# Performance work log

Hardware: AMD Instinct MI355X
Metric: run time of the kernel (lower is better)

## Reference

```python
import jax, jax.numpy as jnp
import numpy as np

N, K, C, S = 32768, 16, 64, 8
EPS = 1e-5

def _bn(x, g, b):
    # BatchNorm1d in training mode: normalize over all axes except channel (last)
    axes = tuple(range(x.ndim - 1))
    m = x.mean(axes, keepdims=True)
    v = x.var(axes, keepdims=True)
    return (x - m) * jax.lax.rsqrt(v + EPS) * g + b

def setup_inputs() -> dict:
    key = jax.random.key(0)
    ks = jax.random.split(key, 24)
    def W(k, i, o):
        return (jax.random.normal(k, (i, o), jnp.float32) * 0.02)
    d = {}
    d['xyz'] = jax.random.normal(ks[0], (N, 3), jnp.float32)
    d['features'] = jax.random.normal(ks[1], (N, C), jnp.float32)
    d['velocities'] = jax.random.normal(ks[2], (N, 1), jnp.float32)
    # q/k/v projections
    d['wq'] = W(ks[3], C, C); d['bq'] = jnp.zeros((C,), jnp.float32)
    d['wk'] = W(ks[4], C, C); d['bk'] = jnp.zeros((C,), jnp.float32)
    d['wv'] = W(ks[5], C, C); d['bv'] = jnp.zeros((C,), jnp.float32)
    # linear_p: Linear(3,3) -> BN(3) -> ReLU -> Linear(3,C)
    d['p1_w'] = W(ks[6], 3, 3); d['p1_b'] = jnp.zeros((3,), jnp.float32)
    d['p_bn_g'] = jnp.ones((3,), jnp.float32); d['p_bn_b'] = jnp.zeros((3,), jnp.float32)
    d['p2_w'] = W(ks[7], 3, C); d['p2_b'] = jnp.zeros((C,), jnp.float32)
    # velocity encoder: Linear(1,1) -> BN(1) -> ReLU -> Linear(1,C)
    d['v1_w'] = W(ks[8], 1, 1); d['v1_b'] = jnp.zeros((1,), jnp.float32)
    d['v_bn_g'] = jnp.ones((1,), jnp.float32); d['v_bn_b'] = jnp.zeros((1,), jnp.float32)
    d['v2_w'] = W(ks[9], 1, C); d['v2_b'] = jnp.zeros((C,), jnp.float32)
    # linear_w: BN(C) -> ReLU -> Linear(C, C//S) -> BN(C//S) -> ReLU -> Linear(C//S, C//S)
    d['w_bn1_g'] = jnp.ones((C,), jnp.float32); d['w_bn1_b'] = jnp.zeros((C,), jnp.float32)
    d['w1_w'] = W(ks[10], C, C // S); d['w1_b'] = jnp.zeros((C // S,), jnp.float32)
    d['w_bn2_g'] = jnp.ones((C // S,), jnp.float32); d['w_bn2_b'] = jnp.zeros((C // S,), jnp.float32)
    d['w2_w'] = W(ks[11], C // S, C // S); d['w2_b'] = jnp.zeros((C // S,), jnp.float32)
    # rho: BN(C) -> ReLU -> Linear(C, C)
    d['rho_bn_g'] = jnp.ones((C,), jnp.float32); d['rho_bn_b'] = jnp.zeros((C,), jnp.float32)
    d['rho_w'] = W(ks[12], C, C); d['rho_b'] = jnp.zeros((C,), jnp.float32)
    # precomputed KNN neighbor indices (coordinate-space and velocity-space)
    d['idx'] = jax.random.randint(ks[13], (N, K), 0, N, jnp.int32)
    d['idx_v'] = jax.random.randint(ks[14], (N, K), 0, N, jnp.int32)
    return d

def reference(xyz, features, velocities, wq, bq, wk, bk, wv, bv,
              p1_w, p1_b, p_bn_g, p_bn_b, p2_w, p2_b,
              v1_w, v1_b, v_bn_g, v_bn_b, v2_w, v2_b,
              w_bn1_g, w_bn1_b, w1_w, w1_b, w_bn2_g, w_bn2_b, w2_w, w2_b,
              rho_bn_g, rho_bn_b, rho_w, rho_b, idx, idx_v):
    x_q = features @ wq + bq                      # [N,C]
    x_k = features @ wk + bk
    x_v = features @ wv + bv
    # queryandgroup: gather neighbors; relative coords prepended for k-path
    p_r = xyz[idx] - xyz[:, None, :]              # [N,K,3]
    x_k_g = x_k[idx]                              # [N,K,C]
    x_v_g = x_v[idx]                              # [N,K,C]
    # positional encoder
    p_enc = jax.nn.relu(_bn(p_r @ p1_w + p1_b, p_bn_g, p_bn_b)) @ p2_w + p2_b   # [N,K,C]
    # velocity encoder (KNN in velocity space)
    v_g = velocities[idx_v]                        # [N,K,1]
    v_enc = jax.nn.relu(_bn(v_g @ v1_w + v1_b, v_bn_g, v_bn_b)) @ v2_w + v2_b   # [N,K,C]
    # subtraction attention scoring
    w = x_k_g - x_q[:, None, :] + (p_enc + v_enc)  # [N,K,C]
    w = jax.nn.relu(_bn(w, w_bn1_g, w_bn1_b)) @ w1_w + w1_b
    w = jax.nn.relu(_bn(w, w_bn2_g, w_bn2_b)) @ w2_w + w2_b   # [N,K,C//S]
    w = jax.nn.softmax(w, axis=1)                  # softmax over neighbors
    # grouped weighted sum with share_planes
    a = (x_v_g + p_enc + v_enc).reshape(N, K, S, C // S)
    out = (a * w[:, :, None, :]).sum(axis=1).reshape(N, C)
    out = out + features
    out = jax.nn.relu(_bn(out, rho_bn_g, rho_bn_b)) @ rho_w + rho_b
    return out
```

## Files before the change

### kernel.cpp

```cpp
#include <hip/hip_runtime.h>

#define NPTS 32768
#define KNN 16
#define CH 64
#define CS 8
#define NKP (NPTS*KNN)
#define EPSBN 1e-5f

#define G1 1024
#define G2 2048
#define G3 2048
#define G4 2048
#define G5 1024

template<int CTRL>
__device__ __forceinline__ float dppf(float x){
  int r = __builtin_amdgcn_update_dpp(0, __float_as_int(x), CTRL, 0xf, 0xf, true);
  return __int_as_float(r);
}
__device__ __forceinline__ float dpp_sum16(float x){
  x += dppf<0xB1>(x); x += dppf<0x4E>(x); x += dppf<0x141>(x); x += dppf<0x140>(x);
  return x;
}
__device__ __forceinline__ float dpp_max16(float x){
  x = fmaxf(x, dppf<0xB1>(x)); x = fmaxf(x, dppf<0x4E>(x));
  x = fmaxf(x, dppf<0x141>(x)); x = fmaxf(x, dppf<0x140>(x));
  return x;
}

struct EncParams {
  float q00,q01,q02,q10,q11,q12,q20,q21,q22;
  float pb0,pb1,pb2;
  float ps0,ps1,ps2, pt0,pt1,pt2;
  float v1w, v1b, vs, vt;
};

__device__ __forceinline__ EncParams load_enc(const float* __restrict__ p1w, const float* __restrict__ p1b,
                                              const float* __restrict__ v1w, const float* __restrict__ v1b,
                                              const float* __restrict__ stats) {
  EncParams P;
  P.q00=p1w[0]; P.q01=p1w[1]; P.q02=p1w[2];
  P.q10=p1w[3]; P.q11=p1w[4]; P.q12=p1w[5];
  P.q20=p1w[6]; P.q21=p1w[7]; P.q22=p1w[8];
  P.pb0=p1b[0]; P.pb1=p1b[1]; P.pb2=p1b[2];
  P.ps0=stats[0]; P.ps1=stats[1]; P.ps2=stats[2];
  P.pt0=stats[3]; P.pt1=stats[4]; P.pt2=stats[5];
  P.v1w=v1w[0]; P.v1b=v1b[0]; P.vs=stats[6]; P.vt=stats[7];
  return P;
}

__device__ __forceinline__ void enc_scalars(const EncParams& P, const float* __restrict__ xyz,
                                            const float* __restrict__ vel, int m, int mv,
                                            float xn0, float xn1, float xn2,
                                            float& ry0, float& ry1, float& ry2, float& rv) {
  float pr0 = xyz[m*3+0]-xn0, pr1 = xyz[m*3+1]-xn1, pr2 = xyz[m*3+2]-xn2;
  float y0 = pr0*P.q00 + pr1*P.q10 + pr2*P.q20 + P.pb0;
  float y1 = pr0*P.q01 + pr1*P.q11 + pr2*P.q21 + P.pb1;
  float y2 = pr0*P.q02 + pr1*P.q12 + pr2*P.q22 + P.pb2;
  ry0 = fmaxf(y0*P.ps0+P.pt0, 0.f);
  ry1 = fmaxf(y1*P.ps1+P.pt1, 0.f);
  ry2 = fmaxf(y2*P.ps2+P.pt2, 0.f);
  float vr = vel[mv]*P.v1w + P.v1b;
  rv = fmaxf(vr*P.vs+P.vt, 0.f);
}

__global__ __launch_bounds__(256, 2) void k1_qkv_stats(
    const float* __restrict__ feat,
    const float* __restrict__ wq, const float* __restrict__ bq,
    const float* __restrict__ wk, const float* __restrict__ bk,
    const float* __restrict__ wv, const float* __restrict__ bv,
    const float* __restrict__ xyz, const float* __restrict__ vel,
    const float* __restrict__ p1w, const float* __restrict__ p1b,
    const float* __restrict__ v1w, const float* __restrict__ v1b,
    const int* __restrict__ idx, const int* __restrict__ idxv,
    float* __restrict__ xq, float* __restrict__ xk, float* __restrict__ xv,
    float* __restrict__ part1)
{
  int tid = threadIdx.x, lane = tid & 63, wave = tid >> 6;
  int nb = blockIdx.x*32;
  if (wave < 3){
    const float* wmat = wave==0? wq : wave==1? wk : wv;
    const float* bias = wave==0? bq : wave==1? bk : bv;
    float* outp = wave==0? xq : wave==1? xk : xv;
    float wcol[64];
    #pragma unroll
    for (int i=0;i<64;i++) wcol[i] = wmat[i*64+lane];
    float bl = bias[lane];
    #pragma unroll
    for (int t=0;t<4;t++){
      float acc[8];
      #pragma unroll
      for (int r=0;r<8;r++) acc[r]=0.f;
      #pragma unroll
      for (int r=0;r<8;r++){
        const float* frow = feat + (size_t)(nb + t*8 + r)*64;
        #pragma unroll
        for (int i=0;i<64;i++) acc[r] += frow[i]*wcol[i];
      }
      #pragma unroll
      for (int r=0;r<8;r++) outp[(size_t)(nb+t*8+r)*64+lane] = acc[r]+bl;
    }
  } else {
    float q00=p1w[0],q01=p1w[1],q02=p1w[2],q10=p1w[3],q11=p1w[4],q12=p1w[5],q20=p1w[6],q21=p1w[7],q22=p1w[8];
    float pb0=p1b[0],pb1=p1b[1],pb2=p1b[2];
    float v1w_=v1w[0], v1b_=v1b[0];
    float s0=0,s1=0,s2=0,sv=0,t0=0,t1=0,t2=0,tv=0;
    #pragma unroll
    for (int rep=0; rep<8; rep++){
      int p = blockIdx.x*512 + rep*64 + lane;
      int n = p >> 4;
      int m = idx[p], mv = idxv[p];
      float xn0=xyz[n*3], xn1=xyz[n*3+1], xn2=xyz[n*3+2];
      float pr0=xyz[m*3]-xn0, pr1=xyz[m*3+1]-xn1, pr2=xyz[m*3+2]-xn2;
      float y0 = pr0*q00+pr1*q10+pr2*q20+pb0;
      float y1 = pr0*q01+pr1*q11+pr2*q21+pb1;
      float y2 = pr0*q02+pr1*q12+pr2*q22+pb2;
      float vr = vel[mv]*v1w_ + v1b_;
      s0+=y0; s1+=y1; s2+=y2; sv+=vr;
      t0+=y0*y0; t1+=y1*y1; t2+=y2*y2; tv+=vr*vr;
    }
    #pragma unroll
    for (int msk=1; msk<64; msk<<=1){
      s0 += __shfl_xor(s0,msk); s1 += __shfl_xor(s1,msk); s2 += __shfl_xor(s2,msk); sv += __shfl_xor(sv,msk);
      t0 += __shfl_xor(t0,msk); t1 += __shfl_xor(t1,msk); t2 += __shfl_xor(t2,msk); tv += __shfl_xor(tv,msk);
    }
    if (lane==0){
      float* pp = &part1[blockIdx.x*8];
      pp[0]=s0; pp[1]=s1; pp[2]=s2; pp[3]=sv;
      pp[4]=t0; pp[5]=t1; pp[6]=t2; pp[7]=tv;
    }
  }
}

__global__ __launch_bounds__(1024) void r1_finalize(
    const float* __restrict__ P, const float* __restrict__ pg, const float* __restrict__ pb,
    const float* __restrict__ vg, const float* __restrict__ vb, float* __restrict__ stats)
{
  constexpr int COLG = 2, NSL = 1024/COLG, ITER = G1/NSL;
  __shared__ float4 red[1024];
  int t = threadIdx.x; int cg = t % COLG, sl = t / COLG;
  float4 acc = make_float4(0.f,0.f,0.f,0.f);
  const float4* P4 = (const float4*)P;
  #pragma unroll
  for (int j=0;j<ITER;j++){
    int i = sl + j*NSL;
    float4 v = P4[i*COLG + cg];
    acc.x+=v.x; acc.y+=v.y; acc.z+=v.z; acc.w+=v.w;
  }
  red[t] = acc; __syncthreads();
  for (int off = NSL/2; off>0; off>>=1){
    if (sl < off){
      float4 o = red[(sl+off)*COLG + cg];
      acc.x+=o.x; acc.y+=o.y; acc.z+=o.z; acc.w+=o.w;
      red[sl*COLG + cg] = acc;
    }
    __syncthreads();
  }
  if (t<4){
    float s = ((float*)red)[t];
    float q = ((float*)red)[4+t];
    float inv = 1.f/(float)NKP;
    float mean=s*inv, var=q*inv-mean*mean;
    float g = (t<3)? pg[t]:vg[0];
    float b = (t<3)? pb[t]:vb[0];
    float sc = g*rsqrtf(var+EPSBN);
    float sh = b - mean*sc;
    if (t<3){ stats[t]=sc; stats[3+t]=sh; } else { stats[6]=sc; stats[7]=sh; }
  }
}

__global__ __launch_bounds__(256) void k1b_renc(
    const float* __restrict__ xyz, const float* __restrict__ vel,
    const float* __restrict__ p1w, const float* __restrict__ p1b,
    const float* __restrict__ v1w, const float* __restrict__ v1b,
    const int* __restrict__ idx, const int* __restrict__ idxv,
    const float* __restrict__ stats, float* __restrict__ renc)
{
  EncParams P = load_enc(p1w,p1b,v1w,v1b,stats);
  int p = blockIdx.x*256 + threadIdx.x;
  int n = p >> 4;
  int m = idx[p], mv = idxv[p];
  float ry0,ry1,ry2,rv;
  enc_scalars(P, xyz, vel, m, mv, xyz[n*3], xyz[n*3+1], xyz[n*3+2], ry0,ry1,ry2,rv);
  ((float4*)renc)[p] = make_float4(ry0,ry1,ry2,rv);
}

template<int NB, int NCH>
__global__ __launch_bounds__(1024) void finalize_bn_t(
    const float* __restrict__ P, float inv,
    const float* __restrict__ g, const float* __restrict__ b,
    float* __restrict__ oscale, float* __restrict__ oshift)
{
  constexpr int COLS = 2*NCH;
  constexpr int COLG = COLS/4;
  constexpr int NSL  = 1024/COLG;
  constexpr int ITER = NB/NSL;
  __shared__ float4 red[1024];
  int t = threadIdx.x; int cg = t % COLG, sl = t / COLG;
  float4 acc = make_float4(0.f,0.f,0.f,0.f);
  const float4* P4 = (const float4*)P;
  #pragma unroll 8
  for (int j=0;j<ITER;j++){
    int i = sl + j*NSL;
    float4 v = P4[i*COLG + cg];
    acc.x+=v.x; acc.y+=v.y; acc.z+=v.z; acc.w+=v.w;
  }
  red[t] = acc; __syncthreads();
  for (int off = NSL/2; off>0; off>>=1){
    if (sl < off){
      float4 o = red[(sl+off)*COLG + cg];
      acc.x+=o.x; acc.y+=o.y; acc.z+=o.z; acc.w+=o.w;
      red[sl*COLG + cg] = acc;
    }
    __syncthreads();
  }
  if (t < NCH){
    float s = ((float*)red)[t];
    float q = ((float*)red)[NCH + t];
    float mean=s*inv, var=q*inv-mean*mean;
    float sc=g[t]*rsqrtf(var+EPSBN);
    oscale[t]=sc; oshift[t]=b[t]-mean*sc;
  }
}

__global__ __launch_bounds__(256) void k2_wstats(
    const int* __restrict__ idx, const float* __restrict__ renc,
    const float* __restrict__ p2w, const float* __restrict__ p2b,
    const float* __restrict__ v2w, const float* __restrict__ v2b,
    const float* __restrict__ xq, const float* __restrict__ xk,
    float* __restrict__ part2)
{
  int tid = threadIdx.x;
  int lane = tid & 63, wave = tid >> 6;
  float A = p2w[lane], B = p2w[64+lane], C2 = p2w[128+lane];
  float D = v2w[lane], E = p2b[lane] + v2b[lane];
  const float4* renc4 = (const float4*)renc;
  float sum=0.f, ssq=0.f;
  int gw = blockIdx.x*4 + wave;
  for (int n0 = gw; n0 < NPTS; n0 += G2*4){
    int nu = __builtin_amdgcn_readfirstlane(n0);
    float xqc = xq[nu*64+lane];
    #pragma unroll 4
    for (int k=0;k<KNN;k++){
      int pu = nu*KNN + k;
      int m = idx[pu];
      float4 rr = renc4[pu];
      float e = rr.x*A + rr.y*B + rr.z*C2 + rr.w*D + E;
      float w = xk[m*64+lane] - xqc + e;
      sum += w; ssq += w*w;
    }
  }
  __shared__ float rs[4][64], rq[4][64];
  rs[wave][lane]=sum; rq[wave][lane]=ssq;
  __syncthreads();
  if (tid < 64){
    float s = rs[0][tid]+rs[1][tid]+rs[2][tid]+rs[3][tid];
    float q = rq[0][tid]+rq[1][tid]+rq[2][tid]+rq[3][tid];
    part2[blockIdx.x*128 + tid] = s;
    part2[blockIdx.x*128 + 64 + tid] = q;
  }
}

__global__ __launch_bounds__(256) void k3_w1(
    const float* __restrict__ p2w, const float* __restrict__ p2b,
    const float* __restrict__ v2w, const float* __restrict__ v2b,
    const float* __restrict__ w1w, const float* __restrict__ w1b,
    const int* __restrict__ idx, const float* __restrict__ renc,
    const float* __restrict__ xq, const float* __restrict__ xk,
    const float* __restrict__ stats,
    float* __restrict__ w1o, float* __restrict__ part3)
{
  __shared__ __attribute__((aligned(16))) float coef[64*20];
  __shared__ float rs[256], rq[256];
  int tid=threadIdx.x;
  if (tid < 64){
    int c = tid;
    int slot = ((c&7)<<3) | (c>>3);
    float* cf = &coef[slot*20];
    cf[0]=p2w[c]; cf[1]=p2w[64+c]; cf[2]=p2w[128+c];
    cf[3]=v2w[c]; cf[4]=p2b[c]+v2b[c];
    cf[5]=stats[8+c]; cf[6]=stats[72+c];
    #pragma unroll
    for (int j=0;j<8;j++) cf[7+j]=w1w[c*8+j];
    #pragma unroll
    for (int j=15;j<20;j++) cf[j]=0.f;
  }
  __syncthreads();
  int lane=tid&63, wave=tid>>6;
  int sl = lane&7, sp = lane>>3;
  bool p4 = (sl&4)==0, p1 = (sl&1)==0, p2 = (sl&2)==0;
  int jmap = (sl&4) | ((sl&1)<<1) | ((sl&2)>>1);
  float w1b_l = w1b[jmap];
  const float4* renc4=(const float4*)renc;
  const float4* xk4=(const float4*)xk;
  const float4* xq4=(const float4*)xq;
  float ssum=0.f, sqq=0.f;
  int gw = blockIdx.x*4 + wave;
  for (int it = gw; it < NKP/32; it += G3*4){
    int pbase = it*32 + sp*4;
    int n = pbase >> 4;
    int4 mi = *(const int4*)&idx[pbase];
    float4 rrs[4] = {renc4[pbase+0], renc4[pbase+1], renc4[pbase+2], renc4[pbase+3]};
    float4 xqa = xq4[n*16 + sl*2], xqb = xq4[n*16 + sl*2 + 1];
    float xqv[8] = {xqa.x,xqa.y,xqa.z,xqa.w, xqb.x,xqb.y,xqb.z,xqb.w};
    float xkv[4][8];
    {
      int mm[4] = {mi.x, mi.y, mi.z, mi.w};
      #pragma unroll
      for (int u=0;u<4;u++){
        float4 a = xk4[mm[u]*16 + sl*2], b = xk4[mm[u]*16 + sl*2 + 1];
        xkv[u][0]=a.x; xkv[u][1]=a.y; xkv[u][2]=a.z; xkv[u][3]=a.w;
        xkv[u][4]=b.x; xkv[u][5]=b.y; xkv[u][6]=b.z; xkv[u][7]=b.w;
      }
    }
    float h[4][8];
    #pragma unroll
    for (int u=0;u<4;u++)
      #pragma unroll
      for (int j=0;j<8;j++) h[u][j]=0.f;
    #pragma unroll
    for (int r=0;r<8;r++){
      const float* cf = &coef[(r*8+sl)*20];
      float4 ca = *(const float4*)(cf+0);
      float4 cb = *(const float4*)(cf+4);
      float4 cc = *(const float4*)(cf+8);
      float4 cd = *(const float4*)(cf+12);
      #pragma unroll
      for (int u=0;u<4;u++){
        float e = rrs[u].x*ca.x + rrs[u].y*ca.y + rrs[u].z*ca.z + rrs[u].w*ca.w + cb.x;
        float w = xkv[u][r] - xqv[r] + e;
        float rw = fmaxf(w*cb.y + cb.z, 0.f);
        h[u][0] += rw*cb.w; h[u][1] += rw*cc.x; h[u][2] += rw*cc.y; h[u][3] += rw*cc.z;
        h[u][4] += rw*cc.w; h[u][5] += rw*cd.x; h[u][6] += rw*cd.y; h[u][7] += rw*cd.z;
      }
    }
    #pragma unroll
    for (int u=0;u<4;u++){
      float g0 = (p4? h[u][0]:h[u][4]) + dppf<0x141>(p4? h[u][4]:h[u][0]);
      float g1 = (p4? h[u][1]:h[u][5]) + dppf<0x141>(p4? h[u][5]:h[u][1]);
      float g2 = (p4? h[u][2]:h[u][6]) + dppf<0x141>(p4? h[u][6]:h[u][2]);
      float g3 = (p4? h[u][3]:h[u][7]) + dppf<0x141>(p4? h[u][7]:h[u][3]);
      float f0 = (p1? g0:g2) + dppf<0xB1>(p1? g2:g0);
      float f1 = (p1? g1:g3) + dppf<0xB1>(p1? g3:g1);
      float S  = (p2? f0:f1) + dppf<0x4E>(p2? f1:f0);
      float o = S + w1b_l;
      w1o[(pbase+u)*8 + jmap] = o;
      ssum += o; sqq += o*o;
    }
  }
  rs[(tid & ~7) | jmap]=ssum; rq[(tid & ~7) | jmap]=sqq;
  __syncthreads();
  if (tid < 8){
    float s=0.f,q=0.f;
    #pragma unroll 8
    for (int i=0;i<32;i++){ s+=rs[i*8+tid]; q+=rq[i*8+tid]; }
    part3[blockIdx.x*16 + tid] = s;
    part3[blockIdx.x*16 + 8 + tid] = q;
  }
}

__global__ __launch_bounds__(256) void k4_agg(
    const float* __restrict__ feat,
    const float* __restrict__ p2w, const float* __restrict__ p2b,
    const float* __restrict__ v2w, const float* __restrict__ v2b,
    const float* __restrict__ w2w, const float* __restrict__ w2b,
    const int* __restrict__ idx, const float* __restrict__ renc,
    const float* __restrict__ xv, const float* __restrict__ w1o,
    const float* __restrict__ stats,
    float* __restrict__ outpre, float* __restrict__ part4)
{
  __shared__ float sm_s[4][16][8];
  __shared__ float rs[4][64], rq[4][64];
  int tid=threadIdx.x, lane=tid&63, wave=tid>>6;
  int kq = lane & 15, jh = lane >> 4;
  float s2[8], t2[8];
  #pragma unroll
  for (int i=0;i<8;i++){ s2[i]=stats[136+i]; t2[i]=stats[144+i]; }
  float w2c0[8], w2c1[8];
  #pragma unroll
  for (int i=0;i<8;i++){ w2c0[i]=w2w[i*8+jh]; w2c1[i]=w2w[i*8+jh+4]; }
  float w2b0=w2b[jh], w2b1=w2b[jh+4];
  float A=p2w[lane], B=p2w[64+lane], C2=p2w[128+lane], D=v2w[lane], E=p2b[lane]+v2b[lane];
  int j = lane & 7;
  const float4* renc4 = (const float4*)renc;
  float sr=0.f, sq2=0.f;
  int gw = blockIdx.x*4 + wave;
  for (int n0 = gw; n0 < NPTS; n0 += G4*4){
    int nu = __builtin_amdgcn_readfirstlane(n0);
    const float* w1p = &w1o[(nu*KNN + kq)*8];
    float4 wa = *(const float4*)w1p;
    float4 wb = *(const float4*)(w1p+4);
    float r0 = fmaxf(wa.x*s2[0]+t2[0],0.f);
    float r1 = fmaxf(wa.y*s2[1]+t2[1],0.f);
    float r2 = fmaxf(wa.z*s2[2]+t2[2],0.f);
    float r3 = fmaxf(wa.w*s2[3]+t2[3],0.f);
    float r4 = fmaxf(wb.x*s2[4]+t2[4],0.f);
    float r5 = fmaxf(wb.y*s2[5]+t2[5],0.f);
    float r6 = fmaxf(wb.z*s2[6]+t2[6],0.f);
    float r7 = fmaxf(wb.w*s2[7]+t2[7],0.f);
    float g0 = r0*w2c0[0]+r1*w2c0[1]+r2*w2c0[2]+r3*w2c0[3]
             + r4*w2c0[4]+r5*w2c0[5]+r6*w2c0[6]+r7*w2c0[7] + w2b0;
    float g1 = r0*w2c1[0]+r1*w2c1[1]+r2*w2c1[2]+r3*w2c1[3]
             + r4*w2c1[4]+r5*w2c1[5]+r6*w2c1[6]+r7*w2c1[7] + w2b1;
    float m0 = dpp_max16(g0), m1 = dpp_max16(g1);
    float e0=__expf(g0-m0), e1=__expf(g1-m1);
    float d0 = dpp_sum16(e0), d1 = dpp_sum16(e1);
    sm_s[wave][kq][jh]   = e0/d0;
    sm_s[wave][kq][jh+4] = e1/d1;
    __asm__ __volatile__("" ::: "memory");
    float acc=0.f;
    #pragma unroll 4
    for (int k=0;k<KNN;k++){
      int pu = nu*KNN+k;
      int m = idx[pu];
      float4 rr = renc4[pu];
      float e = rr.x*A + rr.y*B + rr.z*C2 + rr.w*D + E;
      acc += (xv[m*64+lane] + e) * sm_s[wave][k][j];
    }
    float o = acc + feat[nu*64+lane];
    outpre[nu*64+lane] = o;
    sr += o; sq2 += o*o;
    __asm__ __volatile__("" ::: "memory");
  }
  rs[wave][lane]=sr; rq[wave][lane]=sq2;
  __syncthreads();
  if (tid<64){
    float s=rs[0][tid]+rs[1][tid]+rs[2][tid]+rs[3][tid];
    float q=rq[0][tid]+rq[1][tid]+rq[2][tid]+rq[3][tid];
    part4[blockIdx.x*128+tid]=s;
    part4[blockIdx.x*128+64+tid]=q;
  }
}

__global__ __launch_bounds__(256) void k5_rho(
    const float* __restrict__ outpre, const float* __restrict__ stats,
    const float* __restrict__ rhow, const float* __restrict__ rhob,
    float* __restrict__ out)
{
  __shared__ __attribute__((aligned(16))) float4 lw4[1024];
  __shared__ __attribute__((aligned(16))) float lf[2048];
  float* lw = (float*)lw4;
  int tid=threadIdx.x;
  for (int i=tid;i<1024;i+=256) lw4[i] = ((const float4*)rhow)[i];
  __syncthreads();
  int lane=tid&63, wave=tid>>6;
  int nb = blockIdx.x*32 + wave*8;
  float scl = stats[152+lane], sft = stats[216+lane];
  #pragma unroll
  for (int r=0;r<8;r++){
    float a = outpre[(nb+r)*64+lane];
    lf[wave*512 + r*64 + lane] = fmaxf(a*scl+sft, 0.f);
  }
  float acc[8];
  #pragma unroll
  for (int r=0;r<8;r++) acc[r]=0.f;
  for (int i=0;i<64;i+=4){
    float4 fr[8];
    #pragma unroll
    for (int r=0;r<8;r++) fr[r] = *(const float4*)&lf[wave*512 + r*64 + i];
    #pragma unroll
    for (int ii=0;ii<4;ii++){
      float w_ = lw[(i+ii)*64+lane];
      #pragma unroll
      for (int r=0;r<8;r++){
        float f = ii==0?fr[r].x: ii==1?fr[r].y: ii==2?fr[r].z: fr[r].w;
        acc[r] += f*w_;
      }
    }
  }
  float bl = rhob[lane];
  #pragma unroll
  for (int r=0;r<8;r++) out[(nb+r)*64+lane] = acc[r] + bl;
}

extern "C" void kernel_launch(void* const* d_in, const int* in_sizes, int n_in,
                              void* d_out, int out_size, void* d_ws, size_t ws_size,
                              hipStream_t stream) {
  const float* xyz  = (const float*)d_in[0];
  const float* feat = (const float*)d_in[1];
  const float* vel  = (const float*)d_in[2];
  const float* wq   = (const float*)d_in[3];  const float* bq = (const float*)d_in[4];
  const float* wk   = (const float*)d_in[5];  const float* bk = (const float*)d_in[6];
  const float* wv   = (const float*)d_in[7];  const float* bv = (const float*)d_in[8];
  const float* p1w  = (const float*)d_in[9];  const float* p1b = (const float*)d_in[10];
  const float* pbg  = (const float*)d_in[11]; const float* pbb = (const float*)d_in[12];
  const float* p2w  = (const float*)d_in[13]; const float* p2b = (const float*)d_in[14];
  const float* v1w  = (const float*)d_in[15]; const float* v1b = (const float*)d_in[16];
  const float* vbg  = (const float*)d_in[17]; const float* vbb = (const float*)d_in[18];
  const float* v2w  = (const float*)d_in[19]; const float* v2b = (const float*)d_in[20];
  const float* wbn1g= (const float*)d_in[21]; const float* wbn1b= (const float*)d_in[22];
  const float* w1w  = (const float*)d_in[23]; const float* w1b = (const float*)d_in[24];
  const float* wbn2g= (const float*)d_in[25]; const float* wbn2b= (const float*)d_in[26];
  const float* w2w  = (const float*)d_in[27]; const float* w2b = (const float*)d_in[28];
  const float* rbg  = (const float*)d_in[29]; const float* rbb = (const float*)d_in[30];
  const float* rhow = (const float*)d_in[31]; const float* rhob = (const float*)d_in[32];
  const int* idx    = (const int*)d_in[33];
  const int* idxv   = (const int*)d_in[34];

  float* ws = (float*)d_ws;
  float* xq     = ws;
  float* xk     = xq + (size_t)NPTS*CH;
  float* xv     = xk + (size_t)NPTS*CH;
  float* w1o    = xv + (size_t)NPTS*CH;
  float* outpre = w1o + (size_t)NKP*CS;
  float* renc   = outpre + (size_t)NPTS*CH;
  float* part1  = renc + (size_t)NKP*4;
  float* part2  = part1 + G1*8;
  float* part3  = part2 + (size_t)G2*128;
  float* part4  = part3 + G3*16;
  float* stats  = part4 + (size_t)G4*128;

  k1_qkv_stats<<<dim3(G1), dim3(256), 0, stream>>>(
      feat, wq,bq,wk,bk,wv,bv, xyz, vel, p1w,p1b,v1w,v1b, idx, idxv, xq,xk,xv, part1);
  r1_finalize<<<dim3(1), dim3(1024), 0, stream>>>(part1, pbg,pbb, vbg,vbb, stats);
  k1b_renc<<<dim3(NKP/256), dim3(256), 0, stream>>>(
      xyz, vel, p1w,p1b, v1w,v1b, idx, idxv, stats, renc);
  k2_wstats<<<dim3(G2), dim3(256), 0, stream>>>(
      idx, renc, p2w,p2b,v2w,v2b, xq, xk, part2);
  finalize_bn_t<G2,64><<<dim3(1), dim3(1024), 0, stream>>>(
      part2, 1.f/(float)NKP, wbn1g, wbn1b, stats+8, stats+72);
  k3_w1<<<dim3(G3), dim3(256), 0, stream>>>(
      p2w,p2b,v2w,v2b, w1w,w1b, idx, renc, xq, xk, stats, w1o, part3);
  finalize_bn_t<G3,8><<<dim3(1), dim3(1024), 0, stream>>>(
      part3, 1.f/(float)NKP, wbn2g, wbn2b, stats+136, stats+144);
  k4_agg<<<dim3(G4), dim3(256), 0, stream>>>(
      feat, p2w,p2b,v2w,v2b, w2w,w2b, idx, renc, xv, w1o, stats, outpre, part4);
  finalize_bn_t<G4,64><<<dim3(1), dim3(1024), 0, stream>>>(
      part4, 1.f/(float)NPTS, rbg, rbb, stats+152, stats+216);
  k5_rho<<<dim3(G5), dim3(256), 0, stream>>>(outpre, stats, rhow, rhob, (float*)d_out);

  (void)in_sizes; (void)n_in; (void)out_size; (void)ws_size;
}
```

Measured before the change: 177.1 us.

## Restructure QKV projection to row-per-lane with transposed weights

```diff
diff --git a/kernel.cpp b/kernel.cpp
--- a/kernel.cpp
+++ b/kernel.cpp
@@ -7,7 +7,7 @@
 #define NKP (NPTS*KNN)
 #define EPSBN 1e-5f
 
-#define G1 1024
+#define G1 512
 #define G2 2048
 #define G3 2048
 #define G4 2048
@@ -27,6 +27,11 @@
   x = fmaxf(x, dppf<0x141>(x)); x = fmaxf(x, dppf<0x140>(x));
   return x;
 }
+
+__device__ __forceinline__ float dot4(float4 a, float4 b){
+  return a.x*b.x + a.y*b.y + a.z*b.z + a.w*b.w;
+}
+#define PIN4(v) asm volatile("" : "+v"((v).x), "+v"((v).y), "+v"((v).z), "+v"((v).w))
 
 struct EncParams {
   float q00,q01,q02,q10,q11,q12,q20,q21,q22;
@@ -64,11 +69,20 @@
   rv = fmaxf(vr*P.vs+P.vt, 0.f);
 }
 
-__global__ __launch_bounds__(256, 2) void k1_qkv_stats(
-    const float* __restrict__ feat,
-    const float* __restrict__ wq, const float* __restrict__ bq,
-    const float* __restrict__ wk, const float* __restrict__ bk,
-    const float* __restrict__ wv, const float* __restrict__ bv,
+__global__ __launch_bounds__(256) void k0_wt(
+    const float* __restrict__ wq, const float* __restrict__ wk, const float* __restrict__ wv,
+    float* __restrict__ wT)
+{
+  int t = blockIdx.x*256 + threadIdx.x;
+  int mat = t >> 12, rem = t & 4095;
+  int c = rem >> 6, i = rem & 63;
+  const float* w = mat==0? wq : mat==1? wk : wv;
+  wT[t] = w[i*64 + c];
+}
+
+__global__ __launch_bounds__(256, 2) void k1_gemm_stats(
+    const float* __restrict__ feat, const float* __restrict__ wT,
+    const float* __restrict__ bq, const float* __restrict__ bk, const float* __restrict__ bv,
     const float* __restrict__ xyz, const float* __restrict__ vel,
     const float* __restrict__ p1w, const float* __restrict__ p1b,
     const float* __restrict__ v1w, const float* __restrict__ v1b,
@@ -77,40 +91,43 @@
     float* __restrict__ part1)
 {
   int tid = threadIdx.x, lane = tid & 63, wave = tid >> 6;
-  int nb = blockIdx.x*32;
+  int row = blockIdx.x*64 + lane;
   if (wave < 3){
-    const float* wmat = wave==0? wq : wave==1? wk : wv;
+    const float4* fp = (const float4*)(feat + (size_t)row*64);
+    float4 f0=fp[0], f1=fp[1], f2=fp[2], f3=fp[3], f4=fp[4], f5=fp[5], f6=fp[6], f7=fp[7];
+    float4 f8=fp[8], f9=fp[9], f10=fp[10], f11=fp[11], f12=fp[12], f13=fp[13], f14=fp[14], f15=fp[15];
+    PIN4(f0); PIN4(f1); PIN4(f2); PIN4(f3); PIN4(f4); PIN4(f5); PIN4(f6); PIN4(f7);
+    PIN4(f8); PIN4(f9); PIN4(f10); PIN4(f11); PIN4(f12); PIN4(f13); PIN4(f14); PIN4(f15);
+    const float* wTm = wT + wave*4096;
     const float* bias = wave==0? bq : wave==1? bk : bv;
     float* outp = wave==0? xq : wave==1? xk : xv;
-    float wcol[64];
-    #pragma unroll
-    for (int i=0;i<64;i++) wcol[i] = wmat[i*64+lane];
-    float bl = bias[lane];
-    #pragma unroll
-    for (int t=0;t<4;t++){
-      float acc[8];
+    float4* o4 = (float4*)(outp + (size_t)row*64);
+    #pragma unroll
+    for (int cg=0; cg<8; cg++){
+      float a[8];
       #pragma unroll
-      for (int r=0;r<8;r++) acc[r]=0.f;
-      #pragma unroll
-      for (int r=0;r<8;r++){
-        const float* frow = feat + (size_t)(nb + t*8 + r)*64;
-        #pragma unroll
-        for (int i=0;i<64;i++) acc[r] += frow[i]*wcol[i];
+      for (int u=0; u<8; u++){
+        int c = cg*8+u;
+        const float4* wc4 = (const float4*)(wTm + c*64);
+        float s0 = dot4(f0,wc4[0])  + dot4(f1,wc4[1])  + dot4(f2,wc4[2])  + dot4(f3,wc4[3]);
+        float s1 = dot4(f4,wc4[4])  + dot4(f5,wc4[5])  + dot4(f6,wc4[6])  + dot4(f7,wc4[7]);
+        float s2 = dot4(f8,wc4[8])  + dot4(f9,wc4[9])  + dot4(f10,wc4[10])+ dot4(f11,wc4[11]);
+        float s3 = dot4(f12,wc4[12])+ dot4(f13,wc4[13])+ dot4(f14,wc4[14])+ dot4(f15,wc4[15]);
+        a[u] = (s0+s1)+(s2+s3) + bias[c];
       }
-      #pragma unroll
-      for (int r=0;r<8;r++) outp[(size_t)(nb+t*8+r)*64+lane] = acc[r]+bl;
+      o4[cg*2+0] = make_float4(a[0],a[1],a[2],a[3]);
+      o4[cg*2+1] = make_float4(a[4],a[5],a[6],a[7]);
     }
   } else {
     float q00=p1w[0],q01=p1w[1],q02=p1w[2],q10=p1w[3],q11=p1w[4],q12=p1w[5],q20=p1w[6],q21=p1w[7],q22=p1w[8];
     float pb0=p1b[0],pb1=p1b[1],pb2=p1b[2];
     float v1w_=v1w[0], v1b_=v1b[0];
+    float xn0=xyz[row*3], xn1=xyz[row*3+1], xn2=xyz[row*3+2];
     float s0=0,s1=0,s2=0,sv=0,t0=0,t1=0,t2=0,tv=0;
     #pragma unroll
-    for (int rep=0; rep<8; rep++){
-      int p = blockIdx.x*512 + rep*64 + lane;
-      int n = p >> 4;
+    for (int k=0;k<KNN;k++){
+      int p = row*KNN + k;
       int m = idx[p], mv = idxv[p];
-      float xn0=xyz[n*3], xn1=xyz[n*3+1], xn2=xyz[n*3+2];
       float pr0=xyz[m*3]-xn0, pr1=xyz[m*3+1]-xn1, pr2=xyz[m*3+2]-xn2;
       float y0 = pr0*q00+pr1*q10+pr2*q20+pb0;
       float y1 = pr0*q01+pr1*q11+pr2*q21+pb1;
@@ -132,11 +149,12 @@
   }
 }
 
-__global__ __launch_bounds__(1024) void r1_finalize(
+template<int NB>
+__global__ __launch_bounds__(1024) void r1_finalize_t(
     const float* __restrict__ P, const float* __restrict__ pg, const float* __restrict__ pb,
     const float* __restrict__ vg, const float* __restrict__ vb, float* __restrict__ stats)
 {
-  constexpr int COLG = 2, NSL = 1024/COLG, ITER = G1/NSL;
+  constexpr int COLG = 2, NSL = 1024/COLG, ITER = (NB+NSL-1)/NSL;
   __shared__ float4 red[1024];
   int t = threadIdx.x; int cg = t % COLG, sl = t / COLG;
   float4 acc = make_float4(0.f,0.f,0.f,0.f);
@@ -144,8 +162,10 @@
   #pragma unroll
   for (int j=0;j<ITER;j++){
     int i = sl + j*NSL;
-    float4 v = P4[i*COLG + cg];
-    acc.x+=v.x; acc.y+=v.y; acc.z+=v.z; acc.w+=v.w;
+    if (i < NB){
+      float4 v = P4[i*COLG + cg];
+      acc.x+=v.x; acc.y+=v.y; acc.z+=v.z; acc.w+=v.w;
+    }
   }
   red[t] = acc; __syncthreads();
   for (int off = NSL/2; off>0; off>>=1){
@@ -504,15 +524,17 @@
   float* w1o    = xv + (size_t)NPTS*CH;
   float* outpre = w1o + (size_t)NKP*CS;
   float* renc   = outpre + (size_t)NPTS*CH;
-  float* part1  = renc + (size_t)NKP*4;
+  float* wT     = renc + (size_t)NKP*4;
+  float* part1  = wT + 3*4096;
   float* part2  = part1 + G1*8;
   float* part3  = part2 + (size_t)G2*128;
   float* part4  = part3 + G3*16;
   float* stats  = part4 + (size_t)G4*128;
 
-  k1_qkv_stats<<<dim3(G1), dim3(256), 0, stream>>>(
-      feat, wq,bq,wk,bk,wv,bv, xyz, vel, p1w,p1b,v1w,v1b, idx, idxv, xq,xk,xv, part1);
-  r1_finalize<<<dim3(1), dim3(1024), 0, stream>>>(part1, pbg,pbb, vbg,vbb, stats);
+  k0_wt<<<dim3(48), dim3(256), 0, stream>>>(wq, wk, wv, wT);
+  k1_gemm_stats<<<dim3(G1), dim3(256), 0, stream>>>(
+      feat, wT, bq, bk, bv, xyz, vel, p1w,p1b,v1w,v1b, idx, idxv, xq,xk,xv, part1);
+  r1_finalize_t<G1><<<dim3(1), dim3(1024), 0, stream>>>(part1, pbg,pbb, vbg,vbb, stats);
   k1b_renc<<<dim3(NKP/256), dim3(256), 0, stream>>>(
       xyz, vel, p1w,p1b, v1w,v1b, idx, idxv, stats, renc);
   k2_wstats<<<dim3(G2), dim3(256), 0, stream>>>(
```

Result: slower. 195.3 us (+10.3%).

## Restructure QKV projection to one row per lane with vectorized loads

Applied to the files above, without the earlier changes.

```diff
diff --git a/kernel.cpp b/kernel.cpp
--- a/kernel.cpp
+++ b/kernel.cpp
@@ -7,7 +7,7 @@
 #define NKP (NPTS*KNN)
 #define EPSBN 1e-5f
 
-#define G1 1024
+#define G1 512
 #define G2 2048
 #define G3 2048
 #define G4 2048
@@ -64,7 +64,7 @@
   rv = fmaxf(vr*P.vs+P.vt, 0.f);
 }
 
-__global__ __launch_bounds__(256, 2) void k1_qkv_stats(
+__global__ __launch_bounds__(256) void k1_qkv_stats(
     const float* __restrict__ feat,
     const float* __restrict__ wq, const float* __restrict__ bq,
     const float* __restrict__ wk, const float* __restrict__ bk,
@@ -76,48 +76,60 @@
     float* __restrict__ xq, float* __restrict__ xk, float* __restrict__ xv,
     float* __restrict__ part1)
 {
-  int tid = threadIdx.x, lane = tid & 63, wave = tid >> 6;
-  int nb = blockIdx.x*32;
-  if (wave < 3){
-    const float* wmat = wave==0? wq : wave==1? wk : wv;
-    const float* bias = wave==0? bq : wave==1? bk : bv;
-    float* outp = wave==0? xq : wave==1? xk : xv;
-    float wcol[64];
-    #pragma unroll
-    for (int i=0;i<64;i++) wcol[i] = wmat[i*64+lane];
-    float bl = bias[lane];
-    #pragma unroll
-    for (int t=0;t<4;t++){
-      float acc[8];
+  int tid = threadIdx.x, lane = tid & 63;
+  int wu = __builtin_amdgcn_readfirstlane(tid >> 6);
+  int row = blockIdx.x*64 + lane;
+  if (wu < 3){
+    const float* wmat = wu==0? wq : wu==1? wk : wv;
+    const float* bias = wu==0? bq : wu==1? bk : bv;
+    float* outp = wu==0? xq : wu==1? xk : xv;
+    const float4* fp = (const float4*)(feat + (size_t)row*64);
+    float acc[64];
+    #pragma unroll
+    for (int c=0;c<64;c++) acc[c] = 0.f;
+    for (int i4=0;i4<16;i4++){
+      float4 f = fp[i4];
       #pragma unroll
-      for (int r=0;r<8;r++) acc[r]=0.f;
-      #pragma unroll
-      for (int r=0;r<8;r++){
-        const float* frow = feat + (size_t)(nb + t*8 + r)*64;
+      for (int ii=0;ii<4;ii++){
+        float fv = ii==0?f.x: ii==1?f.y: ii==2?f.z: f.w;
+        const float* wrow = wmat + (i4*4+ii)*64;
         #pragma unroll
-        for (int i=0;i<64;i++) acc[r] += frow[i]*wcol[i];
+        for (int c=0;c<64;c++)
+          acc[c] += fv * wrow[c];
       }
-      #pragma unroll
-      for (int r=0;r<8;r++) outp[(size_t)(nb+t*8+r)*64+lane] = acc[r]+bl;
+    }
+    float4* o4 = (float4*)(outp + (size_t)row*64);
+    #pragma unroll
+    for (int cg=0;cg<16;cg++){
+      o4[cg] = make_float4(acc[cg*4+0]+bias[cg*4+0], acc[cg*4+1]+bias[cg*4+1],
+                           acc[cg*4+2]+bias[cg*4+2], acc[cg*4+3]+bias[cg*4+3]);
     }
   } else {
     float q00=p1w[0],q01=p1w[1],q02=p1w[2],q10=p1w[3],q11=p1w[4],q12=p1w[5],q20=p1w[6],q21=p1w[7],q22=p1w[8];
     float pb0=p1b[0],pb1=p1b[1],pb2=p1b[2];
     float v1w_=v1w[0], v1b_=v1b[0];
+    const int4* ip  = (const int4*)(idx  + (size_t)row*16);
+    const int4* ivp = (const int4*)(idxv + (size_t)row*16);
+    int4 ia[4], iva[4];
+    #pragma unroll
+    for (int j=0;j<4;j++){ ia[j]=ip[j]; iva[j]=ivp[j]; }
+    float xn0=xyz[row*3], xn1=xyz[row*3+1], xn2=xyz[row*3+2];
     float s0=0,s1=0,s2=0,sv=0,t0=0,t1=0,t2=0,tv=0;
     #pragma unroll
-    for (int rep=0; rep<8; rep++){
-      int p = blockIdx.x*512 + rep*64 + lane;
-      int n = p >> 4;
-      int m = idx[p], mv = idxv[p];
-      float xn0=xyz[n*3], xn1=xyz[n*3+1], xn2=xyz[n*3+2];
-      float pr0=xyz[m*3]-xn0, pr1=xyz[m*3+1]-xn1, pr2=xyz[m*3+2]-xn2;
-      float y0 = pr0*q00+pr1*q10+pr2*q20+pb0;
-      float y1 = pr0*q01+pr1*q11+pr2*q21+pb1;
-      float y2 = pr0*q02+pr1*q12+pr2*q22+pb2;
-      float vr = vel[mv]*v1w_ + v1b_;
-      s0+=y0; s1+=y1; s2+=y2; sv+=vr;
-      t0+=y0*y0; t1+=y1*y1; t2+=y2*y2; tv+=vr*vr;
+    for (int j=0;j<4;j++){
+      int mm[4]  = {ia[j].x, ia[j].y, ia[j].z, ia[j].w};
+      int mvv[4] = {iva[j].x, iva[j].y, iva[j].z, iva[j].w};
+      #pragma unroll
+      for (int u=0;u<4;u++){
+        int m = mm[u], mv = mvv[u];
+        float pr0=xyz[m*3]-xn0, pr1=xyz[m*3+1]-xn1, pr2=xyz[m*3+2]-xn2;
+        float y0 = pr0*q00+pr1*q10+pr2*q20+pb0;
+        float y1 = pr0*q01+pr1*q11+pr2*q21+pb1;
+        float y2 = pr0*q02+pr1*q12+pr2*q22+pb2;
+        float vr = vel[mv]*v1w_ + v1b_;
+        s0+=y0; s1+=y1; s2+=y2; sv+=vr;
+        t0+=y0*y0; t1+=y1*y1; t2+=y2*y2; tv+=vr*vr;
+      }
     }
     #pragma unroll
     for (int msk=1; msk<64; msk<<=1){
@@ -132,11 +144,12 @@
   }
 }
 
-__global__ __launch_bounds__(1024) void r1_finalize(
+template<int NB>
+__global__ __launch_bounds__(1024) void r1_finalize_t(
     const float* __restrict__ P, const float* __restrict__ pg, const float* __restrict__ pb,
     const float* __restrict__ vg, const float* __restrict__ vb, float* __restrict__ stats)
 {
-  constexpr int COLG = 2, NSL = 1024/COLG, ITER = G1/NSL;
+  constexpr int COLG = 2, NSL = 1024/COLG, ITER = (NB+NSL-1)/NSL;
   __shared__ float4 red[1024];
   int t = threadIdx.x; int cg = t % COLG, sl = t / COLG;
   float4 acc = make_float4(0.f,0.f,0.f,0.f);
@@ -144,8 +157,10 @@
   #pragma unroll
   for (int j=0;j<ITER;j++){
     int i = sl + j*NSL;
-    float4 v = P4[i*COLG + cg];
-    acc.x+=v.x; acc.y+=v.y; acc.z+=v.z; acc.w+=v.w;
+    if (i < NB){
+      float4 v = P4[i*COLG + cg];
+      acc.x+=v.x; acc.y+=v.y; acc.z+=v.z; acc.w+=v.w;
+    }
   }
   red[t] = acc; __syncthreads();
   for (int off = NSL/2; off>0; off>>=1){
@@ -512,7 +527,7 @@
 
   k1_qkv_stats<<<dim3(G1), dim3(256), 0, stream>>>(
       feat, wq,bq,wk,bk,wv,bv, xyz, vel, p1w,p1b,v1w,v1b, idx, idxv, xq,xk,xv, part1);
-  r1_finalize<<<dim3(1), dim3(1024), 0, stream>>>(part1, pbg,pbb, vbg,vbb, stats);
+  r1_finalize_t<G1><<<dim3(1), dim3(1024), 0, stream>>>(part1, pbg,pbb, vbg,vbb, stats);
   k1b_renc<<<dim3(NKP/256), dim3(256), 0, stream>>>(
       xyz, vel, p1w,p1b, v1w,v1b, idx, idxv, stats, renc);
   k2_wstats<<<dim3(G2), dim3(256), 0, stream>>>(
```

Measured after the change: 159.9 us (median of 2 runs). 9.8% less time.
